# Kernel optimization log

Hardware: AMD Instinct MI355X
Metric: run time of the kernel (lower is better)

Reference implementation:

```python
import jax, jax.numpy as jnp
import numpy as np
from jax import lax

NUM_HEADS = 8
EPS = 1e-12  # F.normalize default eps


def setup_inputs() -> dict:
    key = jax.random.key(0)
    k1, k2, k3, k4 = jax.random.split(key, 4)
    b, c, h, w, d = 2, 128, 48, 48, 48
    x = jax.random.normal(k1, (b, c, h, w, d), dtype=jnp.float32)
    qkv_w = jax.random.normal(k2, (3 * c, c), dtype=jnp.float32) * 0.05
    dw_w = jax.random.normal(k3, (3 * c, 1, 3, 3, 3), dtype=jnp.float32) * 0.05
    proj_w = jax.random.normal(k4, (c, c), dtype=jnp.float32) * 0.05
    temperature = jnp.ones((1, NUM_HEADS, 1, 1), dtype=jnp.float32)
    return {"x": x, "qkv_w": qkv_w, "dw_w": dw_w, "proj_w": proj_w,
            "temperature": temperature}


def _l2_normalize(t):
    # F.normalize(t, dim=-1): t / max(||t||_2, eps)
    n = jnp.sqrt(jnp.sum(t * t, axis=-1, keepdims=True))
    return t / jnp.maximum(n, EPS)


def reference(x, qkv_w, dw_w, proj_w, temperature):
    b, c, h, w, d = x.shape
    dh = c // NUM_HEADS
    N = h * w * d
    # 1x1x1 pointwise conv (c -> 3c), no bias: pure channel GEMM
    qkv = jnp.einsum('oc,bchwd->bohwd', qkv_w, x)
    # depthwise 3x3x3 conv, padding=1, groups=3c
    qkv = lax.conv_general_dilated(
        qkv, dw_w, window_strides=(1, 1, 1), padding=[(1, 1)] * 3,
        dimension_numbers=('NCDHW', 'OIDHW', 'NCDHW'),
        feature_group_count=3 * c)
    q, k, v = jnp.split(qkv, 3, axis=1)
    q = q.reshape(b, NUM_HEADS, dh, N)
    k = k.reshape(b, NUM_HEADS, dh, N)
    v = v.reshape(b, NUM_HEADS, dh, N)
    q = _l2_normalize(q)
    k = _l2_normalize(k)
    # transposed attention: [b,H,dh,dh] score matrix over channels
    attn = jnp.einsum('bhin,bhjn->bhij', q, k) * temperature
    attn = jax.nn.softmax(attn, axis=-1)
    out = jnp.einsum('bhij,bhjn->bhin', attn, v).reshape(b, c, h, w, d)
    # 1x1x1 projection (c -> c), no bias
    return jnp.einsum('oc,bchwd->bohwd', proj_w, out)
```

## Files before the change

kernel.cpp:

```cpp
#include <hip/hip_runtime.h>
#include <hip/hip_bf16.h>
#include <stdint.h>
#include <stddef.h>

#define NSP 110592
#define SD  48
#define SD2 2304
#define CIN 128
#define C3  384
#define NH  8
#define NB  2
#define NQ  84934656ull

typedef __hip_bfloat16 bf16;
typedef __bf16 bf16x8 __attribute__((ext_vector_type(8)));
typedef float  f32x4  __attribute__((ext_vector_type(4)));

#define WOFF_QKVW 0
#define WOFF_DWW  49152
#define WOFF_PROJ 59520
#define WOFF_TEMP 75904
#define WTOTAL    75912

__device__ __forceinline__ float ldb(const bf16* p){ return __bfloat162float(*p); }
__device__ __forceinline__ float b2f(uint16_t u){
    union { float f; uint32_t i; } x; x.i = (uint32_t)u << 16; return x.f;
}
__device__ __forceinline__ uint16_t f2b(float f){
    bf16 h = __float2bfloat16(f); return *(uint16_t*)&h;
}

__global__ void k_sniff(const uint16_t* __restrict__ x16, int* __restrict__ flag)
{
    int t = threadIdx.x; int cnt = 0;
    for (int i = 0; i < 16; ++i) {
        uint16_t b = x16[(size_t)(t * 16 + i) * 2];
        int e = (b >> 7) & 0xFF;
        if (e >= 100 && e <= 140) ++cnt;
    }
    for (int off = 32; off; off >>= 1) cnt += __shfl_down(cnt, off, 64);
    __shared__ int s[4];
    if ((t & 63) == 0) s[t >> 6] = cnt;
    __syncthreads();
    if (t == 0) *flag = (s[0] + s[1] + s[2] + s[3] < 2048) ? 1 : 0;
}

__global__ void k_cvtw(const void* __restrict__ qw, const void* __restrict__ dw,
                       const void* __restrict__ pw, const void* __restrict__ tw,
                       bf16* __restrict__ wbuf, const int* __restrict__ flagp)
{
    int f = *flagp;
    int idx = blockIdx.x * 256 + threadIdx.x;
    if (idx >= WTOTAL) return;
    const void* src; int off;
    if (idx < WOFF_DWW)      { src = qw; off = idx; }
    else if (idx < WOFF_PROJ){ src = dw; off = idx - WOFF_DWW; }
    else if (idx < WOFF_TEMP){ src = pw; off = idx - WOFF_PROJ; }
    else                     { src = tw; off = idx - WOFF_TEMP; }
    float v = f ? ((const float*)src)[off]
                : __bfloat162float(((const bf16*)src)[off]);
    wbuf[idx] = __float2bfloat16(v);
}

__global__ __launch_bounds__(256) void k_gemm_qkv(const bf16* __restrict__ A,
                                                  const void* __restrict__ X,
                                                  bf16* __restrict__ Cout,
                                                  const int* __restrict__ flagp)
{
    __shared__ __align__(16) bf16 lA[128 * CIN];
    __shared__ __align__(16) bf16 lB[128 * CIN];
    int f = *flagp;
    int b = blockIdx.z;
    int bx = blockIdx.x;
    int g = bx / 24, w = bx % 24;
    int nb = g * 8 + (w & 7);
    int mb = w >> 3;
    size_t nbase = (size_t)nb * 128;
    const bf16* gA = A + (size_t)mb * 128 * CIN;
    int t = threadIdx.x;

#pragma unroll
    for (int i = 0; i < 8; ++i) {
        int idx = i * 256 + t;
        int r = idx >> 4, cc = idx & 15;
        *(uint4*)&lA[r * CIN + cc * 8] = *(const uint4*)&gA[r * CIN + cc * 8];
    }

    int cq = t >> 5;
    int nq = t & 31;
    if (f) {
        const float* xb = (const float*)X + (size_t)b * CIN * NSP + nbase;
#pragma unroll
        for (int p = 0; p < 4; ++p) {
            int c0 = p * 32 + cq * 4;
            float4 rv[4];
#pragma unroll
            for (int r = 0; r < 4; ++r)
                rv[r] = *(const float4*)&xb[(size_t)(c0 + r) * NSP + nq * 4];
#pragma unroll
            for (int e = 0; e < 4; ++e) {
                ushort4 o;
                o.x = f2b(((const float*)&rv[0])[e]);
                o.y = f2b(((const float*)&rv[1])[e]);
                o.z = f2b(((const float*)&rv[2])[e]);
                o.w = f2b(((const float*)&rv[3])[e]);
                *(ushort4*)&lB[(nq * 4 + e) * CIN + c0] = o;
            }
        }
    } else {
        const bf16* xb = (const bf16*)X + (size_t)b * CIN * NSP + nbase;
#pragma unroll
        for (int p = 0; p < 4; ++p) {
            int c0 = p * 32 + cq * 4;
            uint2 rv[4];
#pragma unroll
            for (int r = 0; r < 4; ++r)
                rv[r] = *(const uint2*)&xb[(size_t)(c0 + r) * NSP + nq * 4];
#pragma unroll
            for (int e = 0; e < 4; ++e) {
                ushort4 o;
                o.x = (uint16_t)(e < 2 ? (rv[0].x >> (e * 16)) : (rv[0].y >> ((e - 2) * 16)));
                o.y = (uint16_t)(e < 2 ? (rv[1].x >> (e * 16)) : (rv[1].y >> ((e - 2) * 16)));
                o.z = (uint16_t)(e < 2 ? (rv[2].x >> (e * 16)) : (rv[2].y >> ((e - 2) * 16)));
                o.w = (uint16_t)(e < 2 ? (rv[3].x >> (e * 16)) : (rv[3].y >> ((e - 2) * 16)));
                *(ushort4*)&lB[(nq * 4 + e) * CIN + c0] = o;
            }
        }
    }
    __syncthreads();

    int wave = t >> 6, lane = t & 63;
    int wm = (wave & 1) * 64, wn = (wave >> 1) * 64;
    int lr = lane & 15, lq = lane >> 4;
    f32x4 acc[4][4];
#pragma unroll
    for (int mi = 0; mi < 4; ++mi)
#pragma unroll
        for (int ni = 0; ni < 4; ++ni) acc[mi][ni] = (f32x4){0.f, 0.f, 0.f, 0.f};

#pragma unroll
    for (int ks = 0; ks < 4; ++ks) {
        int kof = ks * 32 + lq * 8;
        bf16x8 af[4], bfv[4];
#pragma unroll
        for (int mi = 0; mi < 4; ++mi)
            af[mi] = *(const bf16x8*)&lA[(wm + mi * 16 + lr) * CIN + kof];
#pragma unroll
        for (int ni = 0; ni < 4; ++ni)
            bfv[ni] = *(const bf16x8*)&lB[(wn + ni * 16 + lr) * CIN + kof];
#pragma unroll
        for (int mi = 0; mi < 4; ++mi)
#pragma unroll
            for (int ni = 0; ni < 4; ++ni)
                acc[mi][ni] = __builtin_amdgcn_mfma_f32_16x16x32_bf16(
                    af[mi], bfv[ni], acc[mi][ni], 0, 0, 0);
    }

    size_t cb = ((size_t)b * C3 + (size_t)mb * 128) * NSP + nbase;
    bf16* Cb = Cout + cb;
#pragma unroll
    for (int mi = 0; mi < 4; ++mi)
#pragma unroll
        for (int ni = 0; ni < 4; ++ni)
#pragma unroll
            for (int r = 0; r < 4; ++r)
                Cb[(size_t)(wm + mi * 16 + lq * 4 + r) * NSP + wn + ni * 16 + lr]
                    = __float2bfloat16(acc[mi][ni][r]);
}

__global__ __launch_bounds__(256) void k_gemm_bt(const bf16* __restrict__ A,
                                                 const bf16* __restrict__ BT,
                                                 void* __restrict__ Cout,
                                                 int Mtotal,
                                                 const int* __restrict__ flagp,
                                                 int mblocks)
{
    __shared__ __align__(16) bf16 lA[128 * CIN];
    __shared__ __align__(16) bf16 lB[128 * CIN];
    int b = blockIdx.z;
    int bx = blockIdx.x;
    int mb, nb;
    if (mblocks == 3) {
        int g = bx / 24, w = bx % 24;
        nb = g * 8 + (w & 7);
        mb = w >> 3;
    } else { mb = 0; nb = bx; }
    size_t nbase = (size_t)nb * 128;
    const bf16* gA = A + (size_t)mb * 128 * CIN;
    const bf16* gB = BT + ((size_t)b * NSP + nbase) * CIN;
    int t = threadIdx.x;
#pragma unroll
    for (int i = 0; i < 8; ++i) {
        int off = (i * 256 + t) * 8;
        *(uint4*)&lA[off] = *(const uint4*)&gA[off];
        *(uint4*)&lB[off] = *(const uint4*)&gB[off];
    }
    __syncthreads();

    int wave = t >> 6, lane = t & 63;
    int wm = (wave & 1) * 64, wn = (wave >> 1) * 64;
    int lr = lane & 15, lq = lane >> 4;
    f32x4 acc[4][4];
#pragma unroll
    for (int mi = 0; mi < 4; ++mi)
#pragma unroll
        for (int ni = 0; ni < 4; ++ni) acc[mi][ni] = (f32x4){0.f, 0.f, 0.f, 0.f};

#pragma unroll
    for (int ks = 0; ks < 4; ++ks) {
        int kof = ks * 32 + lq * 8;
        bf16x8 af[4], bfv[4];
#pragma unroll
        for (int mi = 0; mi < 4; ++mi)
            af[mi] = *(const bf16x8*)&lA[(wm + mi * 16 + lr) * CIN + kof];
#pragma unroll
        for (int ni = 0; ni < 4; ++ni)
            bfv[ni] = *(const bf16x8*)&lB[(wn + ni * 16 + lr) * CIN + kof];
#pragma unroll
        for (int mi = 0; mi < 4; ++mi)
#pragma unroll
            for (int ni = 0; ni < 4; ++ni)
                acc[mi][ni] = __builtin_amdgcn_mfma_f32_16x16x32_bf16(
                    af[mi], bfv[ni], acc[mi][ni], 0, 0, 0);
    }

    int f32o = flagp ? *flagp : 0;
    size_t cb = ((size_t)b * Mtotal + (size_t)mb * 128) * NSP + nbase;
    if (f32o) {
        float* Cb = (float*)Cout + cb;
#pragma unroll
        for (int mi = 0; mi < 4; ++mi)
#pragma unroll
            for (int ni = 0; ni < 4; ++ni)
#pragma unroll
                for (int r = 0; r < 4; ++r)
                    Cb[(size_t)(wm + mi * 16 + lq * 4 + r) * NSP + wn + ni * 16 + lr]
                        = acc[mi][ni][r];
    } else {
        bf16* Cb = (bf16*)Cout + cb;
#pragma unroll
        for (int mi = 0; mi < 4; ++mi)
#pragma unroll
            for (int ni = 0; ni < 4; ++ni)
#pragma unroll
                for (int r = 0; r < 4; ++r)
                    Cb[(size_t)(wm + mi * 16 + lq * 4 + r) * NSP + wn + ni * 16 + lr]
                        = __float2bfloat16(acc[mi][ni][r]);
    }
}

#define PLN 3200
__global__ __launch_bounds__(256) void k_dwconv(const bf16* __restrict__ qkv1,
                                                const bf16* __restrict__ dw,
                                                bf16* __restrict__ qkv2,
                                                float* __restrict__ sums)
{
    __shared__ __align__(16) bf16 lds[8 * PLN];
    __shared__ float red[4];
    int bc = blockIdx.x;
    int slab = blockIdx.y;
    int z0 = slab * 6;
    int ch = bc % C3;
    int t = threadIdx.x;
    const bf16* src = qkv1 + (size_t)bc * NSP;
    bf16* dst = qkv2 + (size_t)bc * NSP;

    float wgt[27];
#pragma unroll
    for (int i = 0; i < 27; ++i) wgt[i] = ldb(&dw[ch * 27 + i]);

#pragma unroll
    for (int i = 0; i < 13; ++i) {
        int idx = i * 256 + t;
        if (idx < 3200) *(uint4*)&lds[idx * 8] = (uint4){0, 0, 0, 0};
    }
    __syncthreads();

#pragma unroll
    for (int i = 0; i < 9; ++i) {
        int vidx = i * 256 + t;
        int p = vidx / 288;
        int r = vidx - p * 288;
        int y = r / 6;
        int dg = r - y * 6;
        int zp = z0 - 1 + p;
        if ((unsigned)zp < SD) {
            uint4 v = *(const uint4*)&src[(size_t)zp * SD2 + y * SD + dg * 8];
            *(uint4*)&lds[(p * PLN + (y + 1) * 64 + 8 + dg * 8)] = v;
        }
    }
    __syncthreads();

    float ssq = 0.f;
#pragma unroll 1
    for (int r = 0; r < 3; ++r) {
        int s = r * 256 + t;
        if (s < 576) {
            int y = s / 12;
            int c4 = (s - y * 12) * 4;
            float acc[6][4];
#pragma unroll
            for (int oz = 0; oz < 6; ++oz)
#pragma unroll
                for (int d = 0; d < 4; ++d) acc[oz][d] = 0.f;

#pragma unroll
            for (int pl = 0; pl < 8; ++pl) {
                const uint16_t* P =
                    (const uint16_t*)lds + pl * PLN + y * 64 + 8 + c4;
                float v[3][6];
#pragma unroll
                for (int dy = 0; dy < 3; ++dy) {
                    const uint16_t* R = P + dy * 64;
                    uint2 m = *(const uint2*)R;
                    v[dy][0] = b2f(R[-1]);
                    v[dy][1] = b2f((uint16_t)m.x);
                    v[dy][2] = b2f((uint16_t)(m.x >> 16));
                    v[dy][3] = b2f((uint16_t)m.y);
                    v[dy][4] = b2f((uint16_t)(m.y >> 16));
                    v[dy][5] = b2f(R[4]);
                }
                float p0[4] = {0.f,0.f,0.f,0.f};
                float p1[4] = {0.f,0.f,0.f,0.f};
                float p2[4] = {0.f,0.f,0.f,0.f};
#pragma unroll
                for (int dy = 0; dy < 3; ++dy)
#pragma unroll
                    for (int dd = 0; dd < 3; ++dd) {
                        float w0 = wgt[dy * 3 + dd];
                        float w1 = wgt[9 + dy * 3 + dd];
                        float w2 = wgt[18 + dy * 3 + dd];
#pragma unroll
                        for (int d = 0; d < 4; ++d) {
                            float xv = v[dy][d + dd];
                            if (pl <= 5)            p0[d] += w0 * xv;
                            if (pl >= 1 && pl <= 6) p1[d] += w1 * xv;
                            if (pl >= 2)            p2[d] += w2 * xv;
                        }
                    }
#pragma unroll
                for (int d = 0; d < 4; ++d) {
                    if (pl <= 5)            acc[pl][d]     += p0[d];
                    if (pl >= 1 && pl <= 6) acc[pl - 1][d] += p1[d];
                    if (pl >= 2)            acc[pl - 2][d] += p2[d];
                }
            }
#pragma unroll
            for (int oz = 0; oz < 6; ++oz) {
                uint16_t u0 = f2b(acc[oz][0]), u1 = f2b(acc[oz][1]);
                uint16_t u2 = f2b(acc[oz][2]), u3 = f2b(acc[oz][3]);
                uint2 o;
                o.x = (uint32_t)u0 | ((uint32_t)u1 << 16);
                o.y = (uint32_t)u2 | ((uint32_t)u3 << 16);
                *(uint2*)&dst[(size_t)(z0 + oz) * SD2 + y * SD + c4] = o;
#pragma unroll
                for (int d = 0; d < 4; ++d) ssq += acc[oz][d] * acc[oz][d];
            }
        }
    }

    for (int off = 32; off; off >>= 1) ssq += __shfl_down(ssq, off, 64);
    if ((t & 63) == 0) red[t >> 6] = ssq;
    __syncthreads();
    if (t == 0) atomicAdd(&sums[bc], red[0] + red[1] + red[2] + red[3]);
}

__global__ __launch_bounds__(256) void k_scores(const bf16* __restrict__ qkv2,
                                                float* __restrict__ scores)
{
    int b = blockIdx.z, h = blockIdx.y;
    const bf16* qb = qkv2 + ((size_t)b * C3 + h * 16) * NSP;
    const bf16* kb = qkv2 + ((size_t)b * C3 + 128 + h * 16) * NSP;
    int t = threadIdx.x, w = t >> 6, lane = t & 63;
    int m = lane & 15, q4 = lane >> 4;
    size_t n0 = (size_t)blockIdx.x * 1024 + (size_t)w * 256 + (size_t)q4 * 8;
    const bf16* qp = qb + (size_t)m * NSP + n0;
    const bf16* kp = kb + (size_t)m * NSP + n0;
    f32x4 acc = (f32x4){0.f, 0.f, 0.f, 0.f};
#pragma unroll
    for (int it = 0; it < 8; ++it) {
        bf16x8 a  = *(const bf16x8*)(qp + it * 32);
        bf16x8 bb = *(const bf16x8*)(kp + it * 32);
        acc = __builtin_amdgcn_mfma_f32_16x16x32_bf16(a, bb, acc, 0, 0, 0);
    }
    float* srow = scores + (size_t)(b * NH + h) * 256;
#pragma unroll
    for (int r = 0; r < 4; ++r)
        atomicAdd(&srow[(q4 * 4 + r) * 16 + m], acc[r]);
}

__global__ void k_softmax(const float* __restrict__ scores,
                          const float* __restrict__ sums,
                          const bf16* __restrict__ temp,
                          float* __restrict__ attn)
{
    int t = threadIdx.x;
    int h = (t >> 4) & 7, b = t >> 7;
    float tau = __bfloat162float(temp[h]);
    float invq = 1.f / fmaxf(sqrtf(sums[b * C3 + (t & 127)]), 1e-12f);
    const float* srow = scores + (size_t)t * 16;
    float s[16]; float mx = -3.4e38f;
#pragma unroll
    for (int j = 0; j < 16; ++j) {
        float invk = 1.f / fmaxf(sqrtf(sums[b * C3 + 128 + h * 16 + j]), 1e-12f);
        s[j] = srow[j] * invq * invk * tau;
        mx = fmaxf(mx, s[j]);
    }
    float sum = 0.f;
#pragma unroll
    for (int j = 0; j < 16; ++j) { s[j] = expf(s[j] - mx); sum += s[j]; }
    float inv = 1.f / sum;
    float* arow = attn + (size_t)t * 16;
#pragma unroll
    for (int j = 0; j < 16; ++j) arow[j] = s[j] * inv;
}

__global__ __launch_bounds__(256) void k_av(const bf16* __restrict__ qkv2,
                                            const float* __restrict__ attn,
                                            bf16* __restrict__ outT)
{
    int b = blockIdx.z, h = blockIdx.y;
    const bf16* vb = qkv2 + ((size_t)b * C3 + 256 + h * 16) * NSP;
    __shared__ float at[256];
    int t = threadIdx.x;
    {
        int i = t >> 4, j = t & 15;
        at[j * 16 + i] = attn[(size_t)(b * NH + h) * 256 + t];
    }
    __syncthreads();
    size_t n0 = (size_t)blockIdx.x * 1024 + (size_t)t * 4;
    float acc[16][4];
#pragma unroll
    for (int i = 0; i < 16; ++i)
#pragma unroll
        for (int k = 0; k < 4; ++k) acc[i][k] = 0.f;
#pragma unroll
    for (int j = 0; j < 16; ++j) {
        uint2 raw = *(const uint2*)&vb[(size_t)j * NSP + n0];
        const bf16* rp = (const bf16*)&raw;
        float vf[4];
#pragma unroll
        for (int k = 0; k < 4; ++k) vf[k] = ldb(&rp[k]);
#pragma unroll
        for (int i = 0; i < 16; ++i) {
            float wv = at[j * 16 + i];
#pragma unroll
            for (int k = 0; k < 4; ++k) acc[i][k] += wv * vf[k];
        }
    }
    bf16* ob = outT + ((size_t)b * NSP + n0) * CIN + h * 16;
#pragma unroll
    for (int k = 0; k < 4; ++k) {
        bf16 tmp[16];
#pragma unroll
        for (int i = 0; i < 16; ++i) tmp[i] = __float2bfloat16(acc[i][k]);
        *(uint4*)&ob[(size_t)k * CIN]     = *(uint4*)&tmp[0];
        *(uint4*)&ob[(size_t)k * CIN + 8] = *(uint4*)&tmp[8];
    }
}

extern "C" void kernel_launch(void* const* d_in, const int* in_sizes, int n_in,
                              void* d_out, int out_size, void* d_ws, size_t ws_size,
                              hipStream_t stream)
{
    const void *px = nullptr, *pq = nullptr, *pd = nullptr, *pp = nullptr, *pt = nullptr;
    for (int i = 0; i < n_in; ++i) {
        switch (in_sizes[i]) {
            case 28311552: px = d_in[i]; break;
            case 49152:    pq = d_in[i]; break;
            case 10368:    pd = d_in[i]; break;
            case 16384:    pp = d_in[i]; break;
            case 8:        pt = d_in[i]; break;
        }
    }
    const size_t required = NQ * 4 + (1u << 20);
    if (!px || !pq || !pd || !pp || !pt || ws_size < required) {
        (void)hipMemsetAsync(d_out, 0, (size_t)out_size * 2, stream);
        return;
    }

    char* ws = (char*)d_ws;
    bf16* qkv1 = (bf16*)ws;
    bf16* qkv2 = (bf16*)(ws + NQ * 2);
    char* small = ws + NQ * 4;
    int*   flag   = (int*)small;
    float* sums   = (float*)(small + 256);
    float* scores = (float*)(small + 8192);
    float* attn   = (float*)(small + 24576);
    bf16*  wbuf   = (bf16*)(small + 40960);
    bf16* outT = qkv1;

    (void)hipMemsetAsync(small, 0, 40960, stream);
    k_sniff<<<1, 256, 0, stream>>>((const uint16_t*)px, flag);
    k_cvtw<<<(WTOTAL + 255) / 256, 256, 0, stream>>>(pq, pd, pp, pt, wbuf, flag);
    k_gemm_qkv<<<dim3(864 * 3, 1, NB), 256, 0, stream>>>(
        wbuf + WOFF_QKVW, px, qkv1, flag);
    k_dwconv<<<dim3(NB * C3, 8), 256, 0, stream>>>(qkv1, wbuf + WOFF_DWW, qkv2, sums);
    k_scores<<<dim3(108, NH, NB), 256, 0, stream>>>(qkv2, scores);
    k_softmax<<<1, 256, 0, stream>>>(scores, sums, wbuf + WOFF_TEMP, attn);
    k_av<<<dim3(108, NH, NB), 256, 0, stream>>>(qkv2, attn, outT);
    k_gemm_bt<<<dim3(864, 1, NB), 256, 0, stream>>>(
        wbuf + WOFF_PROJ, outT, d_out, CIN, flag, 1);
}
```

Before: 533.7 us.

## Fold attention matrix into projection weights and fuse AV with output projection

Precomputes a per-batch combined weight W2 = proj_w · blockdiag(attn) in a tiny kernel, then applies it directly to V with a single MFMA GEMM. This removes the separate AV kernel and the write and re-read of the intermediate transposed output tensor. The GEMM now transposes V tiles into LDS itself, using narrower strided loads and scattered LDS stores. The combined weights are rounded to bf16, which changes where rounding happens relative to the original order.

```diff
diff --git a/kernel.cpp b/kernel.cpp
--- a/kernel.cpp
+++ b/kernel.cpp
@@ -166,87 +166,6 @@
             for (int r = 0; r < 4; ++r)
                 Cb[(size_t)(wm + mi * 16 + lq * 4 + r) * NSP + wn + ni * 16 + lr]
                     = __float2bfloat16(acc[mi][ni][r]);
-}
-
-__global__ __launch_bounds__(256) void k_gemm_bt(const bf16* __restrict__ A,
-                                                 const bf16* __restrict__ BT,
-                                                 void* __restrict__ Cout,
-                                                 int Mtotal,
-                                                 const int* __restrict__ flagp,
-                                                 int mblocks)
-{
-    __shared__ __align__(16) bf16 lA[128 * CIN];
-    __shared__ __align__(16) bf16 lB[128 * CIN];
-    int b = blockIdx.z;
-    int bx = blockIdx.x;
-    int mb, nb;
-    if (mblocks == 3) {
-        int g = bx / 24, w = bx % 24;
-        nb = g * 8 + (w & 7);
-        mb = w >> 3;
-    } else { mb = 0; nb = bx; }
-    size_t nbase = (size_t)nb * 128;
-    const bf16* gA = A + (size_t)mb * 128 * CIN;
-    const bf16* gB = BT + ((size_t)b * NSP + nbase) * CIN;
-    int t = threadIdx.x;
-#pragma unroll
-    for (int i = 0; i < 8; ++i) {
-        int off = (i * 256 + t) * 8;
-        *(uint4*)&lA[off] = *(const uint4*)&gA[off];
-        *(uint4*)&lB[off] = *(const uint4*)&gB[off];
-    }
-    __syncthreads();
-
-    int wave = t >> 6, lane = t & 63;
-    int wm = (wave & 1) * 64, wn = (wave >> 1) * 64;
-    int lr = lane & 15, lq = lane >> 4;
-    f32x4 acc[4][4];
-#pragma unroll
-    for (int mi = 0; mi < 4; ++mi)
-#pragma unroll
-        for (int ni = 0; ni < 4; ++ni) acc[mi][ni] = (f32x4){0.f, 0.f, 0.f, 0.f};
-
-#pragma unroll
-    for (int ks = 0; ks < 4; ++ks) {
-        int kof = ks * 32 + lq * 8;
-        bf16x8 af[4], bfv[4];
-#pragma unroll
-        for (int mi = 0; mi < 4; ++mi)
-            af[mi] = *(const bf16x8*)&lA[(wm + mi * 16 + lr) * CIN + kof];
-#pragma unroll
-        for (int ni = 0; ni < 4; ++ni)
-            bfv[ni] = *(const bf16x8*)&lB[(wn + ni * 16 + lr) * CIN + kof];
-#pragma unroll
-        for (int mi = 0; mi < 4; ++mi)
-#pragma unroll
-            for (int ni = 0; ni < 4; ++ni)
-                acc[mi][ni] = __builtin_amdgcn_mfma_f32_16x16x32_bf16(
-                    af[mi], bfv[ni], acc[mi][ni], 0, 0, 0);
-    }
-
-    int f32o = flagp ? *flagp : 0;
-    size_t cb = ((size_t)b * Mtotal + (size_t)mb * 128) * NSP + nbase;
-    if (f32o) {
-        float* Cb = (float*)Cout + cb;
-#pragma unroll
-        for (int mi = 0; mi < 4; ++mi)
-#pragma unroll
-            for (int ni = 0; ni < 4; ++ni)
-#pragma unroll
-                for (int r = 0; r < 4; ++r)
-                    Cb[(size_t)(wm + mi * 16 + lq * 4 + r) * NSP + wn + ni * 16 + lr]
-                        = acc[mi][ni][r];
-    } else {
-        bf16* Cb = (bf16*)Cout + cb;
-#pragma unroll
-        for (int mi = 0; mi < 4; ++mi)
-#pragma unroll
-            for (int ni = 0; ni < 4; ++ni)
-#pragma unroll
-                for (int r = 0; r < 4; ++r)
-                    Cb[(size_t)(wm + mi * 16 + lq * 4 + r) * NSP + wn + ni * 16 + lr]
-                        = __float2bfloat16(acc[mi][ni][r]);
-    }
 }
 
 #define PLN 3200
@@ -415,47 +334,120 @@
     for (int j = 0; j < 16; ++j) arow[j] = s[j] * inv;
 }
 
-__global__ __launch_bounds__(256) void k_av(const bf16* __restrict__ qkv2,
-                                            const float* __restrict__ attn,
-                                            bf16* __restrict__ outT)
-{
-    int b = blockIdx.z, h = blockIdx.y;
-    const bf16* vb = qkv2 + ((size_t)b * C3 + 256 + h * 16) * NSP;
-    __shared__ float at[256];
+__global__ void k_wproj(const bf16* __restrict__ projw,
+                        const float* __restrict__ attn,
+                        bf16* __restrict__ w2)
+{
+    int b = blockIdx.x;
     int t = threadIdx.x;
-    {
-        int i = t >> 4, j = t & 15;
-        at[j * 16 + i] = attn[(size_t)(b * NH + h) * 256 + t];
-    }
-    __syncthreads();
-    size_t n0 = (size_t)blockIdx.x * 1024 + (size_t)t * 4;
-    float acc[16][4];
-#pragma unroll
-    for (int i = 0; i < 16; ++i)
-#pragma unroll
-        for (int k = 0; k < 4; ++k) acc[i][k] = 0.f;
-#pragma unroll
-    for (int j = 0; j < 16; ++j) {
-        uint2 raw = *(const uint2*)&vb[(size_t)j * NSP + n0];
-        const bf16* rp = (const bf16*)&raw;
-        float vf[4];
-#pragma unroll
-        for (int k = 0; k < 4; ++k) vf[k] = ldb(&rp[k]);
-#pragma unroll
-        for (int i = 0; i < 16; ++i) {
-            float wv = at[j * 16 + i];
-#pragma unroll
-            for (int k = 0; k < 4; ++k) acc[i][k] += wv * vf[k];
-        }
-    }
-    bf16* ob = outT + ((size_t)b * NSP + n0) * CIN + h * 16;
-#pragma unroll
-    for (int k = 0; k < 4; ++k) {
-        bf16 tmp[16];
-#pragma unroll
-        for (int i = 0; i < 16; ++i) tmp[i] = __float2bfloat16(acc[i][k]);
-        *(uint4*)&ob[(size_t)k * CIN]     = *(uint4*)&tmp[0];
-        *(uint4*)&ob[(size_t)k * CIN + 8] = *(uint4*)&tmp[8];
+    int co = t >> 1;
+    int h0 = (t & 1) * 4;
+    const float* ab = attn + (size_t)b * NH * 256;
+    bf16* wr = w2 + (size_t)b * CIN * CIN + (size_t)co * CIN;
+#pragma unroll 1
+    for (int h = h0; h < h0 + 4; ++h) {
+        float pw[16];
+#pragma unroll
+        for (int i = 0; i < 16; ++i) pw[i] = ldb(&projw[co * CIN + h * 16 + i]);
+#pragma unroll 1
+        for (int jj = 0; jj < 16; ++jj) {
+            float s = 0.f;
+#pragma unroll
+            for (int i = 0; i < 16; ++i)
+                s += pw[i] * ab[h * 256 + i * 16 + jj];
+            wr[h * 16 + jj] = __float2bfloat16(s);
+        }
+    }
+}
+
+__global__ __launch_bounds__(256) void k_gemm_w2v(const bf16* __restrict__ W2,
+                                                  const bf16* __restrict__ qkv2,
+                                                  void* __restrict__ Cout,
+                                                  const int* __restrict__ flagp)
+{
+    __shared__ __align__(16) bf16 lA[128 * CIN];
+    __shared__ __align__(16) bf16 lB[128 * CIN];
+    int b = blockIdx.z;
+    size_t nbase = (size_t)blockIdx.x * 128;
+    const bf16* gA = W2 + (size_t)b * CIN * CIN;
+    const bf16* vb = qkv2 + ((size_t)b * C3 + 256) * NSP + nbase;
+    int t = threadIdx.x;
+
+#pragma unroll
+    for (int i = 0; i < 8; ++i) {
+        int off = (i * 256 + t) * 8;
+        *(uint4*)&lA[off] = *(const uint4*)&gA[off];
+    }
+
+    int cq = t >> 5, nq = t & 31;
+#pragma unroll
+    for (int p = 0; p < 4; ++p) {
+        int c0 = p * 32 + cq * 4;
+        uint2 rv[4];
+#pragma unroll
+        for (int r = 0; r < 4; ++r)
+            rv[r] = *(const uint2*)&vb[(size_t)(c0 + r) * NSP + nq * 4];
+#pragma unroll
+        for (int e = 0; e < 4; ++e) {
+            ushort4 o;
+            o.x = (uint16_t)(e < 2 ? (rv[0].x >> (e * 16)) : (rv[0].y >> ((e - 2) * 16)));
+            o.y = (uint16_t)(e < 2 ? (rv[1].x >> (e * 16)) : (rv[1].y >> ((e - 2) * 16)));
+            o.z = (uint16_t)(e < 2 ? (rv[2].x >> (e * 16)) : (rv[2].y >> ((e - 2) * 16)));
+            o.w = (uint16_t)(e < 2 ? (rv[3].x >> (e * 16)) : (rv[3].y >> ((e - 2) * 16)));
+            *(ushort4*)&lB[(nq * 4 + e) * CIN + c0] = o;
+        }
+    }
+    __syncthreads();
+
+    int wave = t >> 6, lane = t & 63;
+    int wm = (wave & 1) * 64, wn = (wave >> 1) * 64;
+    int lr = lane & 15, lq = lane >> 4;
+    f32x4 acc[4][4];
+#pragma unroll
+    for (int mi = 0; mi < 4; ++mi)
+#pragma unroll
+        for (int ni = 0; ni < 4; ++ni) acc[mi][ni] = (f32x4){0.f, 0.f, 0.f, 0.f};
+
+#pragma unroll
+    for (int ks = 0; ks < 4; ++ks) {
+        int kof = ks * 32 + lq * 8;
+        bf16x8 af[4], bfv[4];
+#pragma unroll
+        for (int mi = 0; mi < 4; ++mi)
+            af[mi] = *(const bf16x8*)&lA[(wm + mi * 16 + lr) * CIN + kof];
+#pragma unroll
+        for (int ni = 0; ni < 4; ++ni)
+            bfv[ni] = *(const bf16x8*)&lB[(wn + ni * 16 + lr) * CIN + kof];
+#pragma unroll
+        for (int mi = 0; mi < 4; ++mi)
+#pragma unroll
+            for (int ni = 0; ni < 4; ++ni)
+                acc[mi][ni] = __builtin_amdgcn_mfma_f32_16x16x32_bf16(
+                    af[mi], bfv[ni], acc[mi][ni], 0, 0, 0);
+    }
+
+    int f32o = *flagp;
+    size_t cb = ((size_t)b * CIN) * NSP + nbase;
+    if (f32o) {
+        float* Cb = (float*)Cout + cb;
+#pragma unroll
+        for (int mi = 0; mi < 4; ++mi)
+#pragma unroll
+            for (int ni = 0; ni < 4; ++ni)
+#pragma unroll
+                for (int r = 0; r < 4; ++r)
+                    Cb[(size_t)(wm + mi * 16 + lq * 4 + r) * NSP + wn + ni * 16 + lr]
+                        = acc[mi][ni][r];
+    } else {
+        bf16* Cb = (bf16*)Cout + cb;
+#pragma unroll
+        for (int mi = 0; mi < 4; ++mi)
+#pragma unroll
+            for (int ni = 0; ni < 4; ++ni)
+#pragma unroll
+                for (int r = 0; r < 4; ++r)
+                    Cb[(size_t)(wm + mi * 16 + lq * 4 + r) * NSP + wn + ni * 16 + lr]
+                        = __float2bfloat16(acc[mi][ni][r]);
     }
 }
 
@@ -488,7 +480,7 @@
     float* scores = (float*)(small + 8192);
     float* attn   = (float*)(small + 24576);
     bf16*  wbuf   = (bf16*)(small + 40960);
-    bf16* outT = qkv1;
+    bf16*  w2buf  = (bf16*)(small + 196608);
 
     (void)hipMemsetAsync(small, 0, 40960, stream);
     k_sniff<<<1, 256, 0, stream>>>((const uint16_t*)px, flag);
@@ -498,7 +490,6 @@
     k_dwconv<<<dim3(NB * C3, 8), 256, 0, stream>>>(qkv1, wbuf + WOFF_DWW, qkv2, sums);
     k_scores<<<dim3(108, NH, NB), 256, 0, stream>>>(qkv2, scores);
     k_softmax<<<1, 256, 0, stream>>>(scores, sums, wbuf + WOFF_TEMP, attn);
-    k_av<<<dim3(108, NH, NB), 256, 0, stream>>>(qkv2, attn, outT);
-    k_gemm_bt<<<dim3(864, 1, NB), 256, 0, stream>>>(
-        wbuf + WOFF_PROJ, outT, d_out, CIN, flag, 1);
-}
+    k_wproj<<<NB, 256, 0, stream>>>(wbuf + WOFF_PROJ, attn, w2buf);
+    k_gemm_w2v<<<dim3(864, 1, NB), 256, 0, stream>>>(w2buf, qkv2, d_out, flag);
+}
```

Result: no change. 540.2 us (+1.2%).
